# Optimization experiments

Hardware: AMD Instinct MI355X
Metric: run time of the kernel (lower is better)

The kernel has to match this reference:

```python
import jax, jax.numpy as jnp
import numpy as np

B, CH, XL, YL = 512, 1, 64, 64
H = 64                       # num_heads
D = CH * XL * YL             # 4096
F = D // H                   # feature_dim = 64 (== H, required by the mask multiply)


def setup_inputs() -> dict:
    key = jax.random.key(0)
    k1, k2, k3, k4, k5 = jax.random.split(key, 5)
    scale = 1.0 / np.sqrt(D)  # roughly kaiming-ish init for square linears
    return {
        "x": jax.random.normal(k1, (B, CH, XL, YL), dtype=jnp.float32),
        "interface_map": jax.random.uniform(k2, (B, CH, XL, YL), dtype=jnp.float32),
        "Wq": jax.random.normal(k3, (D, D), dtype=jnp.float32) * scale,
        "Wk": jax.random.normal(k4, (D, D), dtype=jnp.float32) * scale,
        "Wv": jax.random.normal(k5, (D, D), dtype=jnp.float32) * scale,
    }


def reference(x, interface_map, Wq, Wk, Wv):
    b = x.shape[0]
    xf = x.reshape(b, D)
    # nn.Linear(bias=False): y = x @ W.T
    q = (xf @ Wq.T).reshape(b, H, F)
    k = (xf @ Wk.T).reshape(b, H, F)
    v = (xf @ Wv.T).reshape(b, H, F)
    inv_sqrt_f = jnp.float32(1.0 / np.sqrt(F))
    qk_t = jnp.einsum("bhf,bgf->bhg", q, k) * inv_sqrt_f           # (B, H, H)
    qk_t = qk_t * interface_map.reshape(b, H, F)                   # multiplicative mask (F == H)
    attention_weights = jax.nn.softmax(qk_t, axis=-1)
    weighted_values = jnp.einsum("bhg,bgf->bhf", attention_weights, v)  # (B, H, F)
    combined = jnp.swapaxes(weighted_values, 1, 2).reshape(b, CH, XL, YL)
    output = x * combined
    return output, attention_weights
```

## Files before the change

### kernel.cpp

```cpp
#include <hip/hip_runtime.h>
#include <cstdint>
#include <cstddef>

typedef __attribute__((ext_vector_type(8))) short short8;
typedef __attribute__((ext_vector_type(4))) float f32x4;

#define NB 512
#define DD 4096
#define NP 12288

__device__ __forceinline__ unsigned pk2(float a, float b) {
    unsigned r;
    asm("v_cvt_pk_bf16_f32 %0, %1, %2" : "=v"(r) : "v"(a), "v"(b));
    return r;
}

__device__ __forceinline__ void gload_lds16(const void* g, void* l) {
    __builtin_amdgcn_global_load_lds((const __attribute__((address_space(1))) void*)g,
                                     (__attribute__((address_space(3))) void*)l, 16, 0, 0);
}

__global__ __launch_bounds__(256) void cvt_bf16_kernel(const float* __restrict__ src,
                                                       unsigned short* __restrict__ dst,
                                                       int n8) {
    int i = blockIdx.x * 256 + threadIdx.x;
    if (i >= n8) return;
    const float4* s = (const float4*)src + (size_t)i * 2;
    float4 a = s[0], b = s[1];
    uint4 r;
    r.x = pk2(a.x, a.y);
    r.y = pk2(a.z, a.w);
    r.z = pk2(b.x, b.y);
    r.w = pk2(b.z, b.w);
    ((uint4*)dst)[i] = r;
}

template<int KS>
__global__ __launch_bounds__(256, 3) void gemm_qkv_kernel(
    const unsigned short* __restrict__ xb,
    const float* __restrict__ w0, const float* __restrict__ w1, const float* __restrict__ w2,
    float* __restrict__ part)
{
    constexpr int KLEN = DD / KS;
    constexpr int NIT = KLEN / 32;
    constexpr int NWG = 96 * 4 * KS;
    constexpr int CPX = NWG / 8;

    const int bid = blockIdx.x;
    const int orig = (bid & 7) * CPX + (bid >> 3);
    const int nt = orig / (4 * KS);
    const int rest = orig - nt * (4 * KS);
    const int mt = rest / KS;
    const int kz = rest - mt * KS;

    const float* W = (nt < 32) ? w0 : ((nt < 64) ? w1 : w2);
    const int ntl = nt & 31;
    const float* Wbase = W + (size_t)(ntl * 128) * DD + kz * KLEN;
    const unsigned short* Abase = xb + (size_t)(mt * 128) * DD + kz * KLEN;
    float* C = part + (size_t)kz * NB * NP;

    __shared__ unsigned short As[2][128 * 32];
    __shared__ unsigned short Bs[2][128 * 32];

    const int t = threadIdx.x;
    const int l = t & 63;
    const int wv = t >> 6;
    const int wr = wv >> 1, wc = wv & 1;

    f32x4 acc[4][4];
    #pragma unroll
    for (int i = 0; i < 4; ++i)
        #pragma unroll
        for (int j = 0; j < 4; ++j)
            acc[i][j] = (f32x4){0.f, 0.f, 0.f, 0.f};

    const int arow0 = (t >> 2);
    const int acol  = (((t & 3) ^ ((t >> 3) & 3)) * 8);
    const int brow = t >> 1, bh = t & 1;
    const float* wrow = Wbase + (size_t)brow * DD + bh * 16;
    const int bws = (t >> 2) & 3;
    char* const bw0 = (char*)(&Bs[0][0]) + brow * 64 + (((2 * bh) ^ bws) * 16);
    char* const bw1 = (char*)(&Bs[0][0]) + brow * 64 + (((2 * bh + 1) ^ bws) * 16);
    const int cx = ((l >> 4) ^ ((l >> 1) & 3));

    float4 bregA[4], bregB[4];

    #define LOADB(br, kt)  { _Pragma("unroll") for (int j = 0; j < 4; ++j) \
                               br[j] = *(const float4*)(wrow + (kt) * 32 + j * 4); }
    #define STAGEA(kt, buf) { _Pragma("unroll") for (int i = 0; i < 2; ++i) \
                               gload_lds16(Abase + (size_t)(i * 64 + arow0) * DD + (kt) * 32 + acol, \
                                           (char*)(&As[buf][0]) + i * 4096 + wv * 1024); }
    #define WRITEB(br, buf) { uint4 q0, q1; \
                              q0.x = pk2(br[0].x, br[0].y); q0.y = pk2(br[0].z, br[0].w); \
                              q0.z = pk2(br[1].x, br[1].y); q0.w = pk2(br[1].z, br[1].w); \
                              q1.x = pk2(br[2].x, br[2].y); q1.y = pk2(br[2].z, br[2].w); \
                              q1.z = pk2(br[3].x, br[3].y); q1.w = pk2(br[3].z, br[3].w); \
                              *(uint4*)(bw0 + (buf) * 8192) = q0; \
                              *(uint4*)(bw1 + (buf) * 8192) = q1; }

    LOADB(bregA, 0);
    STAGEA(0, 0);
    WRITEB(bregA, 0);
    LOADB(bregB, 1);
    __syncthreads();

    #define ITER(cur, nxt, bwr, bld, kt) { \
        if ((kt) + 1 < NIT) STAGEA((kt) + 1, nxt); \
        if ((kt) + 2 < NIT) LOADB(bld, (kt) + 2); \
        short8 af[4], bfr[4]; \
        _Pragma("unroll") for (int fi = 0; fi < 4; ++fi) { \
            int row = wr * 64 + fi * 16 + (l & 15); \
            af[fi] = *(const short8*)((const char*)(&As[cur][0]) + row * 64 + cx * 16); \
        } \
        _Pragma("unroll") for (int fj = 0; fj < 4; ++fj) { \
            int row = wc * 64 + fj * 16 + (l & 15); \
            bfr[fj] = *(const short8*)((const char*)(&Bs[cur][0]) + row * 64 + cx * 16); \
        } \
        _Pragma("unroll") for (int fi = 0; fi < 4; ++fi) \
            _Pragma("unroll") for (int fj = 0; fj < 4; ++fj) \
                acc[fi][fj] = __builtin_amdgcn_mfma_f32_16x16x32_bf16(af[fi], bfr[fj], acc[fi][fj], 0, 0, 0); \
        if ((kt) + 1 < NIT) WRITEB(bwr, nxt); \
        __syncthreads(); \
    }

    for (int kt = 0; kt < NIT; kt += 2) {
        ITER(0, 1, bregB, bregA, kt);
        ITER(1, 0, bregA, bregB, kt + 1);
    }
    #undef ITER
    #undef LOADB
    #undef STAGEA
    #undef WRITEB

    #pragma unroll
    for (int fi = 0; fi < 4; ++fi) {
        int rbase = mt * 128 + wr * 64 + fi * 16 + (l >> 4) * 4;
        #pragma unroll
        for (int fj = 0; fj < 4; ++fj) {
            int col = nt * 128 + wc * 64 + fj * 16 + (l & 15);
            #pragma unroll
            for (int r = 0; r < 4; ++r)
                C[(size_t)(rbase + r) * NP + col] = acc[fi][fj][r];
        }
    }
}

template<int KS>
__global__ __launch_bounds__(256) void attn_kernel(
    const float* __restrict__ part,
    const float* __restrict__ x,
    const float* __restrict__ imap,
    float* __restrict__ dout)
{
    const int b = blockIdx.x;
    const int t = threadIdx.x;
    const int l = t & 63;
    const int wv = t >> 6;

    __shared__ float sq[64 * 68];
    __shared__ float sk[64 * 68];
    __shared__ float sv[64 * 68];

    const float* base0 = part + (size_t)b * NP;
    const float* base1 = part + (size_t)NB * NP + (size_t)b * NP;

    #pragma unroll
    for (int i = 0; i < 4; ++i) {
        int f4 = i * 256 + t;
        int r = f4 >> 4, c = (f4 & 15) * 4;
        float4 q4 = *(const float4*)(base0 + (size_t)f4 * 4);
        float4 k4 = *(const float4*)(base0 + DD + (size_t)f4 * 4);
        float4 v4 = *(const float4*)(base0 + 2 * DD + (size_t)f4 * 4);
        if (KS == 2) {
            float4 a4 = *(const float4*)(base1 + (size_t)f4 * 4);
            float4 b4 = *(const float4*)(base1 + DD + (size_t)f4 * 4);
            float4 c4 = *(const float4*)(base1 + 2 * DD + (size_t)f4 * 4);
            q4.x += a4.x; q4.y += a4.y; q4.z += a4.z; q4.w += a4.w;
            k4.x += b4.x; k4.y += b4.y; k4.z += b4.z; k4.w += b4.w;
            v4.x += c4.x; v4.y += c4.y; v4.z += c4.z; v4.w += c4.w;
        }
        *(float4*)(&sq[r * 68 + c]) = q4;
        *(float4*)(&sk[r * 68 + c]) = k4;
        *(float4*)(&sv[r * 68 + c]) = v4;
    }
    __syncthreads();

    float accs[16];
    #pragma unroll
    for (int i = 0; i < 16; ++i) accs[i] = 0.f;
    #pragma unroll 4
    for (int f4 = 0; f4 < 16; ++f4) {
        float4 kvv = *(const float4*)(&sk[l * 68 + f4 * 4]);
        #pragma unroll
        for (int i = 0; i < 16; ++i) {
            int h = i * 4 + wv;
            float4 qv = *(const float4*)(&sq[h * 68 + f4 * 4]);
            accs[i] = fmaf(qv.x, kvv.x, fmaf(qv.y, kvv.y, fmaf(qv.z, kvv.z, fmaf(qv.w, kvv.w, accs[i]))));
        }
    }
    __syncthreads();
    #pragma unroll
    for (int i = 0; i < 16; ++i) {
        int h = i * 4 + wv;
        float m = imap[(size_t)b * DD + h * 64 + l];
        sk[h * 65 + l] = accs[i] * 0.125f * m;
    }
    __syncthreads();

    {
        int h = t >> 2, j = t & 3;
        float e[16];
        float mx = -3.0e38f;
        #pragma unroll
        for (int q2 = 0; q2 < 16; ++q2) {
            e[q2] = sk[h * 65 + j * 16 + q2];
            mx = fmaxf(mx, e[q2]);
        }
        mx = fmaxf(mx, __shfl_xor(mx, 1));
        mx = fmaxf(mx, __shfl_xor(mx, 2));
        float s = 0.f;
        #pragma unroll
        for (int q2 = 0; q2 < 16; ++q2) { e[q2] = __expf(e[q2] - mx); s += e[q2]; }
        s += __shfl_xor(s, 1);
        s += __shfl_xor(s, 2);
        float invs = 1.0f / s;
        float* aw = dout + (size_t)NB * DD + (size_t)b * DD + h * 64 + j * 16;
        #pragma unroll
        for (int q2 = 0; q2 < 16; q2 += 4) {
            float4 w4 = {e[q2] * invs, e[q2 + 1] * invs, e[q2 + 2] * invs, e[q2 + 3] * invs};
            *(float4*)(aw + q2) = w4;
            sk[h * 65 + j * 16 + q2 + 0] = w4.x;
            sk[h * 65 + j * 16 + q2 + 1] = w4.y;
            sk[h * 65 + j * 16 + q2 + 2] = w4.z;
            sk[h * 65 + j * 16 + q2 + 3] = w4.w;
        }
    }
    __syncthreads();

    float pacc[16];
    #pragma unroll
    for (int i = 0; i < 16; ++i) pacc[i] = 0.f;
    #pragma unroll 4
    for (int g = 0; g < 64; ++g) {
        float p = sk[l * 65 + g];
        const float4* vr = (const float4*)(&sv[g * 68 + wv * 16]);
        float4 v0 = vr[0], v1 = vr[1], v2 = vr[2], v3 = vr[3];
        pacc[0]  = fmaf(p, v0.x, pacc[0]);
        pacc[1]  = fmaf(p, v0.y, pacc[1]);
        pacc[2]  = fmaf(p, v0.z, pacc[2]);
        pacc[3]  = fmaf(p, v0.w, pacc[3]);
        pacc[4]  = fmaf(p, v1.x, pacc[4]);
        pacc[5]  = fmaf(p, v1.y, pacc[5]);
        pacc[6]  = fmaf(p, v1.z, pacc[6]);
        pacc[7]  = fmaf(p, v1.w, pacc[7]);
        pacc[8]  = fmaf(p, v2.x, pacc[8]);
        pacc[9]  = fmaf(p, v2.y, pacc[9]);
        pacc[10] = fmaf(p, v2.z, pacc[10]);
        pacc[11] = fmaf(p, v2.w, pacc[11]);
        pacc[12] = fmaf(p, v3.x, pacc[12]);
        pacc[13] = fmaf(p, v3.y, pacc[13]);
        pacc[14] = fmaf(p, v3.z, pacc[14]);
        pacc[15] = fmaf(p, v3.w, pacc[15]);
    }
    const size_t ob = (size_t)b * DD + (size_t)(wv * 16) * 64 + l;
    #pragma unroll
    for (int ii = 0; ii < 16; ++ii) {
        size_t o = ob + (size_t)ii * 64;
        dout[o] = x[o] * pacc[ii];
    }
}

extern "C" void kernel_launch(void* const* d_in, const int* in_sizes, int n_in,
                              void* d_out, int out_size, void* d_ws, size_t ws_size,
                              hipStream_t stream) {
    const float* x  = (const float*)d_in[0];
    const float* im = (const float*)d_in[1];
    const float* Wq = (const float*)d_in[2];
    const float* Wk = (const float*)d_in[3];
    const float* Wv = (const float*)d_in[4];
    float* out = (float*)d_out;

    unsigned short* xb = (unsigned short*)d_ws;
    float* part = (float*)((char*)d_ws + (size_t)NB * DD * 2);

    const size_t need2 = (size_t)NB * DD * 2 + 2ull * NB * NP * 4;
    const int KS = (ws_size >= need2) ? 2 : 1;

    cvt_bf16_kernel<<<dim3((NB * DD / 8 + 255) / 256), dim3(256), 0, stream>>>(x, xb, NB * DD / 8);

    if (KS == 2) {
        gemm_qkv_kernel<2><<<dim3(96 * 4 * 2), dim3(256), 0, stream>>>(xb, Wq, Wk, Wv, part);
        attn_kernel<2><<<dim3(NB), dim3(256), 0, stream>>>(part, x, im, out);
    } else {
        gemm_qkv_kernel<1><<<dim3(96 * 4 * 1), dim3(256), 0, stream>>>(xb, Wq, Wk, Wv, part);
        attn_kernel<1><<<dim3(NB), dim3(256), 0, stream>>>(part, x, im, out);
    }
}
```

Before: 141.7 us.

## Load weight fragments straight to registers, skip LDS staging of B

The GEMM no longer stages the fp32 weights through LDS. Each wave now loads its own 32-column slice of W directly into registers in MFMA fragment layout and converts it to bf16 there. The A tile uses a 4-deep LDS ring with prefetch two steps ahead, and explicit vmcnt waits, barriers and setprio replace __syncthreads. Each wave covers all 128 rows times 32 columns, so every wave reads the whole A tile from LDS, and the global W loads are now strided 16-row fragments with less coalescing.

```diff
diff --git a/kernel.cpp b/kernel.cpp
--- a/kernel.cpp
+++ b/kernel.cpp
@@ -55,89 +55,87 @@
 
     const float* W = (nt < 32) ? w0 : ((nt < 64) ? w1 : w2);
     const int ntl = nt & 31;
-    const float* Wbase = W + (size_t)(ntl * 128) * DD + kz * KLEN;
     const unsigned short* Abase = xb + (size_t)(mt * 128) * DD + kz * KLEN;
     float* C = part + (size_t)kz * NB * NP;
 
-    __shared__ unsigned short As[2][128 * 32];
-    __shared__ unsigned short Bs[2][128 * 32];
+    __shared__ unsigned short As[4][128 * 32];
 
     const int t = threadIdx.x;
     const int l = t & 63;
     const int wv = t >> 6;
-    const int wr = wv >> 1, wc = wv & 1;
-
-    f32x4 acc[4][4];
-    #pragma unroll
-    for (int i = 0; i < 4; ++i)
-        #pragma unroll
-        for (int j = 0; j < 4; ++j)
+
+    f32x4 acc[8][2];
+    #pragma unroll
+    for (int i = 0; i < 8; ++i)
+        #pragma unroll
+        for (int j = 0; j < 2; ++j)
             acc[i][j] = (f32x4){0.f, 0.f, 0.f, 0.f};
 
     const int arow0 = (t >> 2);
     const int acol  = (((t & 3) ^ ((t >> 3) & 3)) * 8);
-    const int brow = t >> 1, bh = t & 1;
-    const float* wrow = Wbase + (size_t)brow * DD + bh * 16;
-    const int bws = (t >> 2) & 3;
-    char* const bw0 = (char*)(&Bs[0][0]) + brow * 64 + (((2 * bh) ^ bws) * 16);
-    char* const bw1 = (char*)(&Bs[0][0]) + brow * 64 + (((2 * bh + 1) ^ bws) * 16);
     const int cx = ((l >> 4) ^ ((l >> 1) & 3));
 
-    float4 bregA[4], bregB[4];
-
-    #define LOADB(br, kt)  { _Pragma("unroll") for (int j = 0; j < 4; ++j) \
-                               br[j] = *(const float4*)(wrow + (kt) * 32 + j * 4); }
+    const float* wsrc = W + (size_t)(ntl * 128 + wv * 32 + (l & 15)) * DD + kz * KLEN + (l >> 4) * 8;
+
+    float4 bank0[2][2], bank1[2][2];
+
+    #define LOADB(bk, kt) { _Pragma("unroll") for (int fj = 0; fj < 2; ++fj) \
+                              _Pragma("unroll") for (int h = 0; h < 2; ++h) \
+                                bk[fj][h] = *(const float4*)(wsrc + (size_t)(fj * 16) * DD + (kt) * 32 + h * 4); }
     #define STAGEA(kt, buf) { _Pragma("unroll") for (int i = 0; i < 2; ++i) \
                                gload_lds16(Abase + (size_t)(i * 64 + arow0) * DD + (kt) * 32 + acol, \
                                            (char*)(&As[buf][0]) + i * 4096 + wv * 1024); }
-    #define WRITEB(br, buf) { uint4 q0, q1; \
-                              q0.x = pk2(br[0].x, br[0].y); q0.y = pk2(br[0].z, br[0].w); \
-                              q0.z = pk2(br[1].x, br[1].y); q0.w = pk2(br[1].z, br[1].w); \
-                              q1.x = pk2(br[2].x, br[2].y); q1.y = pk2(br[2].z, br[2].w); \
-                              q1.z = pk2(br[3].x, br[3].y); q1.w = pk2(br[3].z, br[3].w); \
-                              *(uint4*)(bw0 + (buf) * 8192) = q0; \
-                              *(uint4*)(bw1 + (buf) * 8192) = q1; }
-
-    LOADB(bregA, 0);
+
+    #define BODY(kt, BK, PF_OK, VMC) { \
+        short8 bfr[2]; \
+        _Pragma("unroll") for (int fj = 0; fj < 2; ++fj) { \
+            union { uint4 u; short8 s; } cv; \
+            cv.u.x = pk2(BK[fj][0].x, BK[fj][0].y); \
+            cv.u.y = pk2(BK[fj][0].z, BK[fj][0].w); \
+            cv.u.z = pk2(BK[fj][1].x, BK[fj][1].y); \
+            cv.u.w = pk2(BK[fj][1].z, BK[fj][1].w); \
+            bfr[fj] = cv.s; \
+        } \
+        if (PF_OK) { STAGEA((kt) + 2, ((kt) + 2) & 3); LOADB(BK, (kt) + 2); } \
+        __builtin_amdgcn_s_setprio(1); \
+        _Pragma("unroll") for (int fi = 0; fi < 8; ++fi) { \
+            int row = fi * 16 + (l & 15); \
+            short8 af = *(const short8*)((const char*)(&As[(kt) & 3][0]) + row * 64 + cx * 16); \
+            acc[fi][0] = __builtin_amdgcn_mfma_f32_16x16x32_bf16(af, bfr[0], acc[fi][0], 0, 0, 0); \
+            acc[fi][1] = __builtin_amdgcn_mfma_f32_16x16x32_bf16(af, bfr[1], acc[fi][1], 0, 0, 0); \
+        } \
+        __builtin_amdgcn_s_setprio(0); \
+        asm volatile("s_waitcnt vmcnt(" #VMC ") lgkmcnt(0)" ::: "memory"); \
+        __builtin_amdgcn_sched_barrier(0); \
+        __builtin_amdgcn_s_barrier(); \
+        __builtin_amdgcn_sched_barrier(0); \
+    }
+
     STAGEA(0, 0);
-    WRITEB(bregA, 0);
-    LOADB(bregB, 1);
-    __syncthreads();
-
-    #define ITER(cur, nxt, bwr, bld, kt) { \
-        if ((kt) + 1 < NIT) STAGEA((kt) + 1, nxt); \
-        if ((kt) + 2 < NIT) LOADB(bld, (kt) + 2); \
-        short8 af[4], bfr[4]; \
-        _Pragma("unroll") for (int fi = 0; fi < 4; ++fi) { \
-            int row = wr * 64 + fi * 16 + (l & 15); \
-            af[fi] = *(const short8*)((const char*)(&As[cur][0]) + row * 64 + cx * 16); \
-        } \
-        _Pragma("unroll") for (int fj = 0; fj < 4; ++fj) { \
-            int row = wc * 64 + fj * 16 + (l & 15); \
-            bfr[fj] = *(const short8*)((const char*)(&Bs[cur][0]) + row * 64 + cx * 16); \
-        } \
-        _Pragma("unroll") for (int fi = 0; fi < 4; ++fi) \
-            _Pragma("unroll") for (int fj = 0; fj < 4; ++fj) \
-                acc[fi][fj] = __builtin_amdgcn_mfma_f32_16x16x32_bf16(af[fi], bfr[fj], acc[fi][fj], 0, 0, 0); \
-        if ((kt) + 1 < NIT) WRITEB(bwr, nxt); \
-        __syncthreads(); \
-    }
-
-    for (int kt = 0; kt < NIT; kt += 2) {
-        ITER(0, 1, bregB, bregA, kt);
-        ITER(1, 0, bregA, bregB, kt + 1);
-    }
-    #undef ITER
+    STAGEA(1, 1);
+    LOADB(bank0, 0);
+    LOADB(bank1, 1);
+    asm volatile("s_waitcnt vmcnt(0) lgkmcnt(0)" ::: "memory");
+    __builtin_amdgcn_s_barrier();
+    __builtin_amdgcn_sched_barrier(0);
+
+    for (int kt = 0; kt + 2 < NIT; kt += 2) {
+        BODY(kt,     bank0, true, 6);
+        BODY(kt + 1, bank1, true, 6);
+    }
+    BODY(NIT - 2, bank0, false, 0);
+    BODY(NIT - 1, bank1, false, 0);
+
+    #undef BODY
     #undef LOADB
     #undef STAGEA
-    #undef WRITEB
-
-    #pragma unroll
-    for (int fi = 0; fi < 4; ++fi) {
-        int rbase = mt * 128 + wr * 64 + fi * 16 + (l >> 4) * 4;
-        #pragma unroll
-        for (int fj = 0; fj < 4; ++fj) {
-            int col = nt * 128 + wc * 64 + fj * 16 + (l & 15);
+
+    #pragma unroll
+    for (int fi = 0; fi < 8; ++fi) {
+        int rbase = mt * 128 + fi * 16 + (l >> 4) * 4;
+        #pragma unroll
+        for (int fj = 0; fj < 2; ++fj) {
+            int col = nt * 128 + wv * 32 + fj * 16 + (l & 15);
             #pragma unroll
             for (int r = 0; r < 4; ++r)
                 C[(size_t)(rbase + r) * NP + col] = acc[fi][fj][r];
```

Result: slower. 169.4 us (+19.5%).
